# Kernel tuning notes

Measured on AMD Instinct MI355X. Metric: run time of the kernel, lower is better.

## Reference

```python
import jax, jax.numpy as jnp
import numpy as np

B, Q, S, T, H = 8, 64, 64, 64, 768
NH, HD = 12, 64  # head_num, head_dim


def setup_inputs() -> dict:
    key = jax.random.key(0)
    k1, k2, k3, k4, k5, k6, k7 = jax.random.split(key, 7)
    ini_q = jax.random.normal(k1, (B, Q, H), dtype=jnp.float32)
    ini_k = jax.random.normal(k2, (B, S, T, H), dtype=jnp.float32)
    mask = jax.random.randint(k3, (B, S, T), 0, 2).astype(jnp.float32)  # 1 = masked
    # learned params (Linear weights stored as [in, out] for x @ W)
    sc = 1.0 / np.sqrt(H)
    Wq = jax.random.normal(k4, (H, H), dtype=jnp.float32) * sc
    Wkv = jax.random.normal(k5, (H, H), dtype=jnp.float32) * sc
    Wo = jax.random.normal(k6, (H, H), dtype=jnp.float32) * sc
    bo = jax.random.normal(k7, (H,), dtype=jnp.float32) * 0.02
    return {"ini_q": ini_q, "ini_k": ini_k, "mask": mask,
            "Wq": Wq, "Wkv": Wkv, "Wo": Wo, "bo": bo}


def reference(ini_q, ini_k, mask, Wq, Wkv, Wo, bo):
    batch, q_num, _ = ini_q.shape
    _, s_num, t_num, _ = ini_k.shape
    scale = 1.0 / np.sqrt(HD)
    q = (ini_q @ Wq).reshape(batch, q_num, NH, HD)
    kv = (ini_k @ Wkv).reshape(batch, s_num, t_num, NH, HD)  # k == v
    # [b, h, q, s, t]
    scores = jnp.einsum('bqhd,bsthd->bhqst', q, kv) * scale
    scores = scores + mask[:, None, None, :, :] * -10000.0
    alpha = jax.nn.softmax(scores, axis=4)  # dropout is identity in eval
    res = jnp.einsum('bhqst,bsthd->bqshd', alpha, kv).reshape(batch, q_num, s_num, NH * HD)
    return res @ Wo + bo
```

## Files before the change

kernel.cpp:

```cpp
#include <hip/hip_runtime.h>
#include <stdint.h>


typedef __bf16 bf16_t;
typedef __attribute__((ext_vector_type(8))) __bf16 bf16x8;
typedef __attribute__((ext_vector_type(4))) __bf16 bf16x4;
typedef __attribute__((ext_vector_type(4))) float f32x4;

#define HDIM 768

__device__ __forceinline__ void gload16(const bf16_t* g, bf16_t* l) {
  __builtin_amdgcn_global_load_lds(
      (const __attribute__((address_space(1))) void*)g,
      (__attribute__((address_space(3))) void*)l, 16, 0, 0);
}

__global__ __launch_bounds__(256) void splitT3_kernel(
    const float* __restrict__ W0, const float* __restrict__ W1,
    const float* __restrict__ W2,
    bf16_t* __restrict__ h0, bf16_t* __restrict__ l0,
    bf16_t* __restrict__ h1, bf16_t* __restrict__ l1,
    bf16_t* __restrict__ h2, bf16_t* __restrict__ l2) {
  const int kt = blockIdx.x * 64, nt = blockIdx.y * 64, ws = blockIdx.z;
  const float* W = ws == 0 ? W0 : (ws == 1 ? W1 : W2);
  bf16_t* H = ws == 0 ? h0 : (ws == 1 ? h1 : h2);
  bf16_t* L = ws == 0 ? l0 : (ws == 1 ? l1 : l2);
  __shared__ bf16_t Th[64 * 72], Tl[64 * 72];
  const int tid = threadIdx.x;
  const int r0 = tid >> 4, c0 = (tid & 15) * 4;
#pragma unroll
  for (int rg = 0; rg < 4; ++rg) {
    const int r = r0 + rg * 16;
    const float4 v = *(const float4*)&W[(size_t)(kt + r) * HDIM + nt + c0];
    const float vv[4] = {v.x, v.y, v.z, v.w};
#pragma unroll
    for (int e = 0; e < 4; ++e) {
      const bf16_t hb = (bf16_t)vv[e];
      Th[(c0 + e) * 72 + r] = hb;
      Tl[(c0 + e) * 72 + r] = (bf16_t)(vv[e] - (float)hb);
    }
  }
  __syncthreads();
  const int n = tid >> 2, kc = (tid & 3) * 16;
  bf16x8 oh[2], ol[2];
#pragma unroll
  for (int e = 0; e < 16; ++e) {
    oh[e >> 3][e & 7] = Th[n * 72 + kc + e];
    ol[e >> 3][e & 7] = Tl[n * 72 + kc + e];
  }
  const size_t ob = (size_t)(nt + n) * HDIM + kt + kc;
  *(bf16x8*)&H[ob] = oh[0];
  *(bf16x8*)&H[ob + 8] = oh[1];
  *(bf16x8*)&L[ob] = ol[0];
  *(bf16x8*)&L[ob + 8] = ol[1];
}

template <int EPI, bool AF32>
__global__ __launch_bounds__(256) void gemm_kernel(
    const float* __restrict__ Agf,
    const bf16_t* __restrict__ Agh, const bf16_t* __restrict__ Agl,
    const bf16_t* __restrict__ Bgh, const bf16_t* __restrict__ Bgl,
    bf16_t* __restrict__ Ch, bf16_t* __restrict__ Cl,
    bf16_t* __restrict__ CNh, bf16_t* __restrict__ CNl,
    float* __restrict__ Cf, const float* __restrict__ bias) {
  __shared__ bf16_t sAh[128 * 32], sAl[128 * 32];
  __shared__ bf16_t sBh[128 * 32], sBl[128 * 32];
  const int nwg = gridDim.x;
  const int cpx = nwg >> 3;
  const int g = blockIdx.x;
  const int wg = (g & 7) * cpx + (g >> 3);
  const int bn = wg % 6, bm = wg / 6;
  const int tid = threadIdx.x, lane = tid & 63, w = tid >> 6;
  const int wr = (w >> 1) * 64, wc = (w & 1) * 64;
  const int l15 = lane & 15, l4 = lane >> 4;
  f32x4 acc[4][4] = {};

  for (int kt = 0; kt < 24; ++kt) {
    const int k0 = kt * 32;
    __syncthreads();
    if constexpr (AF32) {
#pragma unroll
      for (int j = 0; j < 4; ++j) {
        const int c = tid + j * 256;
        const int row = c >> 3, cg = c & 7;
        const float4 v4 =
            *(const float4*)&Agf[(size_t)(bm * 128 + row) * HDIM + k0 + cg * 4];
        const float vv[4] = {v4.x, v4.y, v4.z, v4.w};
        bf16x4 hv, lv;
#pragma unroll
        for (int e = 0; e < 4; ++e) {
          const bf16_t hb = (bf16_t)vv[e];
          hv[e] = hb;
          lv[e] = (bf16_t)(vv[e] - (float)hb);
        }
        const int off =
            row * 32 + (((cg >> 1) ^ ((row >> 1) & 3)) * 8) + (cg & 1) * 4;
        *(bf16x4*)&sAh[off] = hv;
        *(bf16x4*)&sAl[off] = lv;
      }
    } else {
#pragma unroll
      for (int j = 0; j < 2; ++j) {
        const int c0 = j * 256 + w * 64;
        const int c = c0 + lane;
        const int row = c >> 2, slot = c & 3;
        const size_t ga = (size_t)(bm * 128 + row) * HDIM + k0 +
                          ((slot ^ ((row >> 1) & 3)) * 8);
        gload16(&Agh[ga], &sAh[c0 * 8]);
        gload16(&Agl[ga], &sAl[c0 * 8]);
      }
    }
#pragma unroll
    for (int j = 0; j < 2; ++j) {
      const int c0 = j * 256 + w * 64;
      const int c = c0 + lane;
      const int row = c >> 2, slot = c & 3;
      const size_t gb = (size_t)(bn * 128 + row) * HDIM + k0 +
                        ((slot ^ ((row >> 1) & 3)) * 8);
      gload16(&Bgh[gb], &sBh[c0 * 8]);
      gload16(&Bgl[gb], &sBl[c0 * 8]);
    }
    __syncthreads();
    bf16x8 a_h[4], a_l[4], b_h[4], b_l[4];
#pragma unroll
    for (int m = 0; m < 4; ++m) {
      const int rowa = wr + m * 16 + l15;
      const int ra = rowa * 32 + ((l4 ^ ((rowa >> 1) & 3)) * 8);
      a_h[m] = *(const bf16x8*)&sAh[ra];
      a_l[m] = *(const bf16x8*)&sAl[ra];
      const int rowb = wc + m * 16 + l15;
      const int rb = rowb * 32 + ((l4 ^ ((rowb >> 1) & 3)) * 8);
      b_h[m] = *(const bf16x8*)&sBh[rb];
      b_l[m] = *(const bf16x8*)&sBl[rb];
    }
#pragma unroll
    for (int m = 0; m < 4; ++m)
#pragma unroll
      for (int n = 0; n < 4; ++n) {
        acc[m][n] = __builtin_amdgcn_mfma_f32_16x16x32_bf16(a_h[m], b_h[n], acc[m][n], 0, 0, 0);
        acc[m][n] = __builtin_amdgcn_mfma_f32_16x16x32_bf16(a_h[m], b_l[n], acc[m][n], 0, 0, 0);
        acc[m][n] = __builtin_amdgcn_mfma_f32_16x16x32_bf16(a_l[m], b_h[n], acc[m][n], 0, 0, 0);
      }
  }
#pragma unroll
  for (int m = 0; m < 4; ++m)
#pragma unroll
    for (int n = 0; n < 4; ++n) {
      const int row0 = bm * 128 + wr + m * 16 + l4 * 4;
      const int col = bn * 128 + wc + n * 16 + l15;
      if constexpr (EPI == 1) {
        const float bv = bias[col];
#pragma unroll
        for (int j = 0; j < 4; ++j)
          Cf[(size_t)(row0 + j) * HDIM + col] = acc[m][n][j] + bv;
      } else if constexpr (EPI == 0) {
#pragma unroll
        for (int j = 0; j < 4; ++j) {
          const float v = acc[m][n][j];
          const bf16_t hb = (bf16_t)v;
          Ch[(size_t)(row0 + j) * HDIM + col] = hb;
          Cl[(size_t)(row0 + j) * HDIM + col] = (bf16_t)(v - (float)hb);
        }
      } else {
        const int b = row0 >> 12, s = (row0 >> 6) & 63, t0 = row0 & 63;
        const int hh = col >> 6, d = col & 63;
        const size_t base = ((size_t)((b * 64 + s) * 12 + hh)) * 4096;
#pragma unroll
        for (int j = 0; j < 4; ++j) {
          const float v = acc[m][n][j];
          const bf16_t hb = (bf16_t)v;
          CNh[base + (t0 + j) * 64 + d] = hb;
          CNl[base + (t0 + j) * 64 + d] = (bf16_t)(v - (float)hb);
        }
      }
    }
}

__global__ __launch_bounds__(256, 3) void attn_kernel(
    const bf16_t* __restrict__ qh, const bf16_t* __restrict__ ql,
    const bf16_t* __restrict__ kvNh, const bf16_t* __restrict__ kvNl,
    const float* __restrict__ mask,
    bf16_t* __restrict__ resh, bf16_t* __restrict__ resl) {
  const int sq = blockIdx.x, hh = blockIdx.y, b = blockIdx.z;
  const int s0 = sq * 8;
  const int tid = threadIdx.x, lane = tid & 63, w = tid >> 6;
  const int l15 = lane & 15, l4 = lane >> 4;
  __shared__ bf16_t Kh[64 * 64], Kl[64 * 64];
  __shared__ bf16_t VTh[64 * 72], VTl[64 * 72];
  __shared__ bf16_t Ph[64 * 68], Pl[64 * 68];
  __shared__ float mk[8 * 64];

  {
    const int i2 = tid * 2;
    const float2 mv = *(const float2*)
        &mask[((size_t)(b * 64 + s0 + (i2 >> 6))) * 64 + (i2 & 63)];
    mk[i2] = mv.x * -10000.0f;
    mk[i2 + 1] = mv.y * -10000.0f;
  }

  const size_t qbase = ((size_t)(b * 64 + w * 16 + l15)) * HDIM + hh * 64;
  bf16x8 qf_h[2], qf_l[2];
#pragma unroll
  for (int ks = 0; ks < 2; ++ks) {
    qf_h[ks] = *(const bf16x8*)&qh[qbase + ks * 32 + l4 * 8];
    qf_l[ks] = *(const bf16x8*)&ql[qbase + ks * 32 + l4 * 8];
  }

  const size_t hb0 = ((size_t)((b * 64 + s0) * 12 + hh)) * 4096;
  const size_t SSTR = 12 * 4096;

  bf16x8 nxh[2], nxl[2];
  auto load_next = [&](int sn) {
#pragma unroll
    for (int j = 0; j < 2; ++j) {
      const int c = j * 256 + tid;
      const size_t src = hb0 + (size_t)sn * SSTR + (c >> 3) * 64 + (c & 7) * 8;
      nxh[j] = *(const bf16x8*)&kvNh[src];
      nxl[j] = *(const bf16x8*)&kvNl[src];
    }
  };
  auto write_K = [&]() {
#pragma unroll
    for (int j = 0; j < 2; ++j) {
      const int c = j * 256 + tid;
      const int t = c >> 3, sl = c & 7;
      const int off = t * 64 + ((sl ^ (t & 7)) * 8);
      *(bf16x8*)&Kh[off] = nxh[j];
      *(bf16x8*)&Kl[off] = nxl[j];
    }
  };

  load_next(0);
  write_K();
  __syncthreads();

  const int q = w * 16 + l15;
  for (int si = 0; si < 8; ++si) {
    if (si < 7) load_next(si + 1);

    f32x4 St[4] = {};
#pragma unroll
    for (int ks = 0; ks < 2; ++ks) {
#pragma unroll
      for (int mf = 0; mf < 4; ++mf) {
        const int t = mf * 16 + l15;
        const int off = t * 64 + (((ks * 4 + l4) ^ (t & 7)) * 8);
        const bf16x8 kh8 = *(const bf16x8*)&Kh[off];
        const bf16x8 kl8 = *(const bf16x8*)&Kl[off];
        St[mf] = __builtin_amdgcn_mfma_f32_16x16x32_bf16(kh8, qf_h[ks], St[mf], 0, 0, 0);
        St[mf] = __builtin_amdgcn_mfma_f32_16x16x32_bf16(kh8, qf_l[ks], St[mf], 0, 0, 0);
        St[mf] = __builtin_amdgcn_mfma_f32_16x16x32_bf16(kl8, qf_h[ks], St[mf], 0, 0, 0);
      }
    }

    {
      const int t = lane, sw = t & 7;
#pragma unroll
      for (int ri = 0; ri < 2; ++ri) {
        const int phys = (w * 2 + ri) ^ sw;
        const bf16x8 vh = *(const bf16x8*)&Kh[t * 64 + phys * 8];
        const bf16x8 vl = *(const bf16x8*)&Kl[t * 64 + phys * 8];
        const int d0 = w * 16 + ri * 8;
#pragma unroll
        for (int e = 0; e < 8; ++e) {
          VTh[(d0 + e) * 72 + t] = vh[e];
          VTl[(d0 + e) * 72 + t] = vl[e];
        }
      }
    }

    float p[16];
    float mx = -1e30f;
#pragma unroll
    for (int mf = 0; mf < 4; ++mf)
#pragma unroll
      for (int j = 0; j < 4; ++j) {
        const float v = St[mf][j] * 0.125f + mk[si * 64 + mf * 16 + l4 * 4 + j];
        p[mf * 4 + j] = v;
        mx = fmaxf(mx, v);
      }
    mx = fmaxf(mx, __shfl_xor(mx, 16));
    mx = fmaxf(mx, __shfl_xor(mx, 32));
    float sum = 0.f;
#pragma unroll
    for (int i = 0; i < 16; ++i) {
      const float e = __expf(p[i] - mx);
      p[i] = e;
      sum += e;
    }
    sum += __shfl_xor(sum, 16);
    sum += __shfl_xor(sum, 32);
    const float inv = 1.0f / sum;

#pragma unroll
    for (int mf = 0; mf < 4; ++mf) {
      bf16x4 hv, lv;
#pragma unroll
      for (int j = 0; j < 4; ++j) {
        const float v = p[mf * 4 + j] * inv;
        const bf16_t hb = (bf16_t)v;
        hv[j] = hb;
        lv[j] = (bf16_t)(v - (float)hb);
      }
      *(bf16x4*)&Ph[q * 68 + mf * 16 + l4 * 4] = hv;
      *(bf16x4*)&Pl[q * 68 + mf * 16 + l4 * 4] = lv;
    }
    __syncthreads();

    if (si < 7) write_K();

    f32x4 O[4] = {};
#pragma unroll
    for (int ks = 0; ks < 2; ++ks) {
      const bf16x8 pa = *(const bf16x8*)&Ph[q * 68 + ks * 32 + l4 * 8];
      const bf16x8 pb = *(const bf16x8*)&Pl[q * 68 + ks * 32 + l4 * 8];
#pragma unroll
      for (int nf = 0; nf < 4; ++nf) {
        const int d = nf * 16 + l15;
        const bf16x8 vh = *(const bf16x8*)&VTh[d * 72 + ks * 32 + l4 * 8];
        const bf16x8 vl = *(const bf16x8*)&VTl[d * 72 + ks * 32 + l4 * 8];
        O[nf] = __builtin_amdgcn_mfma_f32_16x16x32_bf16(pa, vh, O[nf], 0, 0, 0);
        O[nf] = __builtin_amdgcn_mfma_f32_16x16x32_bf16(pa, vl, O[nf], 0, 0, 0);
        O[nf] = __builtin_amdgcn_mfma_f32_16x16x32_bf16(pb, vh, O[nf], 0, 0, 0);
      }
    }

#pragma unroll
    for (int nf = 0; nf < 4; ++nf)
#pragma unroll
      for (int j = 0; j < 4; ++j) {
        const int qo = w * 16 + l4 * 4 + j;
        const size_t idx =
            ((size_t)((b * 64 + qo) * 64 + s0 + si)) * HDIM + hh * 64 + nf * 16 + l15;
        const float v = O[nf][j];
        const bf16_t hb = (bf16_t)v;
        resh[idx] = hb;
        resl[idx] = (bf16_t)(v - (float)hb);
      }
    __syncthreads();
  }
}

extern "C" void kernel_launch(void* const* d_in, const int* in_sizes, int n_in,
                              void* d_out, int out_size, void* d_ws, size_t ws_size,
                              hipStream_t stream) {
  const float* ini_q = (const float*)d_in[0];
  const float* ini_k = (const float*)d_in[1];
  const float* mask = (const float*)d_in[2];
  const float* Wq = (const float*)d_in[3];
  const float* Wkv = (const float*)d_in[4];
  const float* Wo = (const float*)d_in[5];
  const float* bo = (const float*)d_in[6];
  float* out = (float*)d_out;

  const size_t SQ = 512ull * HDIM;
  const size_t SK = 32768ull * HDIM;
  const size_t SW = 768ull * HDIM;

  char* p = (char*)d_ws;
  auto carve = [&](size_t bytes) {
    char* r = p;
    p += (bytes + 255) & ~(size_t)255;
    return r;
  };
  bf16_t* wq_h = (bf16_t*)carve(SW * 2);
  bf16_t* wq_l = (bf16_t*)carve(SW * 2);
  bf16_t* wkv_h = (bf16_t*)carve(SW * 2);
  bf16_t* wkv_l = (bf16_t*)carve(SW * 2);
  bf16_t* wo_h = (bf16_t*)carve(SW * 2);
  bf16_t* wo_l = (bf16_t*)carve(SW * 2);
  bf16_t* q_h = (bf16_t*)carve(SQ * 2);
  bf16_t* q_l = (bf16_t*)carve(SQ * 2);
  bf16_t* kvN_h = (bf16_t*)carve(SK * 2);
  bf16_t* kvN_l = (bf16_t*)carve(SK * 2);
  bf16_t* res_h = (bf16_t*)carve(SK * 2);
  bf16_t* res_l = (bf16_t*)carve(SK * 2);
  if ((size_t)(p - (char*)d_ws) > ws_size) return;

  splitT3_kernel<<<dim3(12, 12, 3), 256, 0, stream>>>(
      Wq, Wkv, Wo, wq_h, wq_l, wkv_h, wkv_l, wo_h, wo_l);

  gemm_kernel<0, true><<<dim3(24), 256, 0, stream>>>(
      ini_q, nullptr, nullptr, wq_h, wq_l, q_h, q_l, nullptr, nullptr,
      nullptr, nullptr);
  gemm_kernel<2, true><<<dim3(1536), 256, 0, stream>>>(
      ini_k, nullptr, nullptr, wkv_h, wkv_l, nullptr, nullptr, kvN_h, kvN_l,
      nullptr, nullptr);
  attn_kernel<<<dim3(8, 12, 8), 256, 0, stream>>>(
      q_h, q_l, kvN_h, kvN_l, mask, res_h, res_l);
  gemm_kernel<1, false><<<dim3(1536), 256, 0, stream>>>(
      nullptr, res_h, res_l, wo_h, wo_l, nullptr, nullptr, nullptr, nullptr,
      out, bo);
}
```

Measured before the change: 506.5 us.

## Pre-split fp32 activations to bf16 hi/lo and double-buffer GEMM LDS staging

Adds a standalone split kernel that converts ini_q and ini_k into bf16 hi/lo pairs before the GEMMs, so every GEMM A operand can be loaded straight into LDS with global_load_lds instead of being converted from fp32 inside the k-loop. The GEMM then double-buffers its LDS tiles, issuing the next k-tile's loads before running MFMAs on the current one, with one barrier per iteration. The trade-off is an extra full pass over the large ini_k tensor (read fp32, write two bf16 arrays) and double the GEMM's LDS footprint, which may lower occupancy. The res buffers alias the ik buffers to save workspace; this is safe only because attention runs after the KV GEMM.

```diff
diff --git a/kernel.cpp b/kernel.cpp
--- a/kernel.cpp
+++ b/kernel.cpp
@@ -13,6 +13,23 @@
   __builtin_amdgcn_global_load_lds(
       (const __attribute__((address_space(1))) void*)g,
       (__attribute__((address_space(3))) void*)l, 16, 0, 0);
+}
+
+__global__ __launch_bounds__(256) void split4_kernel(const float* __restrict__ x,
+                                                     bf16_t* __restrict__ h,
+                                                     bf16_t* __restrict__ l) {
+  const int i = blockIdx.x * 256 + threadIdx.x;
+  const float4 v = ((const float4*)x)[i];
+  const float vv[4] = {v.x, v.y, v.z, v.w};
+  bf16x4 hv, lv;
+#pragma unroll
+  for (int e = 0; e < 4; ++e) {
+    const bf16_t hb = (bf16_t)vv[e];
+    hv[e] = hb;
+    lv[e] = (bf16_t)(vv[e] - (float)hb);
+  }
+  ((bf16x4*)h)[i] = hv;
+  ((bf16x4*)l)[i] = lv;
 }
 
 __global__ __launch_bounds__(256) void splitT3_kernel(
@@ -55,16 +72,15 @@
   *(bf16x8*)&L[ob + 8] = ol[1];
 }
 
-template <int EPI, bool AF32>
+template <int EPI>
 __global__ __launch_bounds__(256) void gemm_kernel(
-    const float* __restrict__ Agf,
     const bf16_t* __restrict__ Agh, const bf16_t* __restrict__ Agl,
     const bf16_t* __restrict__ Bgh, const bf16_t* __restrict__ Bgl,
     bf16_t* __restrict__ Ch, bf16_t* __restrict__ Cl,
     bf16_t* __restrict__ CNh, bf16_t* __restrict__ CNl,
     float* __restrict__ Cf, const float* __restrict__ bias) {
-  __shared__ bf16_t sAh[128 * 32], sAl[128 * 32];
-  __shared__ bf16_t sBh[128 * 32], sBl[128 * 32];
+  __shared__ bf16_t sA[2][2][128 * 32];
+  __shared__ bf16_t sB[2][2][128 * 32];
   const int nwg = gridDim.x;
   const int cpx = nwg >> 3;
   const int g = blockIdx.x;
@@ -75,63 +91,40 @@
   const int l15 = lane & 15, l4 = lane >> 4;
   f32x4 acc[4][4] = {};
 
-  for (int kt = 0; kt < 24; ++kt) {
+  auto stage = [&](int buf, int kt) {
     const int k0 = kt * 32;
-    __syncthreads();
-    if constexpr (AF32) {
-#pragma unroll
-      for (int j = 0; j < 4; ++j) {
-        const int c = tid + j * 256;
-        const int row = c >> 3, cg = c & 7;
-        const float4 v4 =
-            *(const float4*)&Agf[(size_t)(bm * 128 + row) * HDIM + k0 + cg * 4];
-        const float vv[4] = {v4.x, v4.y, v4.z, v4.w};
-        bf16x4 hv, lv;
-#pragma unroll
-        for (int e = 0; e < 4; ++e) {
-          const bf16_t hb = (bf16_t)vv[e];
-          hv[e] = hb;
-          lv[e] = (bf16_t)(vv[e] - (float)hb);
-        }
-        const int off =
-            row * 32 + (((cg >> 1) ^ ((row >> 1) & 3)) * 8) + (cg & 1) * 4;
-        *(bf16x4*)&sAh[off] = hv;
-        *(bf16x4*)&sAl[off] = lv;
-      }
-    } else {
-#pragma unroll
-      for (int j = 0; j < 2; ++j) {
-        const int c0 = j * 256 + w * 64;
-        const int c = c0 + lane;
-        const int row = c >> 2, slot = c & 3;
-        const size_t ga = (size_t)(bm * 128 + row) * HDIM + k0 +
-                          ((slot ^ ((row >> 1) & 3)) * 8);
-        gload16(&Agh[ga], &sAh[c0 * 8]);
-        gload16(&Agl[ga], &sAl[c0 * 8]);
-      }
-    }
 #pragma unroll
     for (int j = 0; j < 2; ++j) {
       const int c0 = j * 256 + w * 64;
       const int c = c0 + lane;
       const int row = c >> 2, slot = c & 3;
-      const size_t gb = (size_t)(bn * 128 + row) * HDIM + k0 +
-                        ((slot ^ ((row >> 1) & 3)) * 8);
-      gload16(&Bgh[gb], &sBh[c0 * 8]);
-      gload16(&Bgl[gb], &sBl[c0 * 8]);
-    }
-    __syncthreads();
+      const int soff = ((slot ^ ((row >> 1) & 3)) * 8);
+      const size_t ga = (size_t)(bm * 128 + row) * HDIM + k0 + soff;
+      gload16(&Agh[ga], &sA[buf][0][c0 * 8]);
+      gload16(&Agl[ga], &sA[buf][1][c0 * 8]);
+      const size_t gb = (size_t)(bn * 128 + row) * HDIM + k0 + soff;
+      gload16(&Bgh[gb], &sB[buf][0][c0 * 8]);
+      gload16(&Bgl[gb], &sB[buf][1][c0 * 8]);
+    }
+  };
+
+  stage(0, 0);
+  __syncthreads();
+  int cur = 0;
+
+  for (int kt = 0; kt < 24; ++kt) {
+    if (kt < 23) stage(cur ^ 1, kt + 1);
     bf16x8 a_h[4], a_l[4], b_h[4], b_l[4];
 #pragma unroll
     for (int m = 0; m < 4; ++m) {
       const int rowa = wr + m * 16 + l15;
       const int ra = rowa * 32 + ((l4 ^ ((rowa >> 1) & 3)) * 8);
-      a_h[m] = *(const bf16x8*)&sAh[ra];
-      a_l[m] = *(const bf16x8*)&sAl[ra];
+      a_h[m] = *(const bf16x8*)&sA[cur][0][ra];
+      a_l[m] = *(const bf16x8*)&sA[cur][1][ra];
       const int rowb = wc + m * 16 + l15;
       const int rb = rowb * 32 + ((l4 ^ ((rowb >> 1) & 3)) * 8);
-      b_h[m] = *(const bf16x8*)&sBh[rb];
-      b_l[m] = *(const bf16x8*)&sBl[rb];
+      b_h[m] = *(const bf16x8*)&sB[cur][0][rb];
+      b_l[m] = *(const bf16x8*)&sB[cur][1][rb];
     }
 #pragma unroll
     for (int m = 0; m < 4; ++m)
@@ -141,7 +134,10 @@
         acc[m][n] = __builtin_amdgcn_mfma_f32_16x16x32_bf16(a_h[m], b_l[n], acc[m][n], 0, 0, 0);
         acc[m][n] = __builtin_amdgcn_mfma_f32_16x16x32_bf16(a_l[m], b_h[n], acc[m][n], 0, 0, 0);
       }
-  }
+    __syncthreads();
+    cur ^= 1;
+  }
+
 #pragma unroll
   for (int m = 0; m < 4; ++m)
 #pragma unroll
@@ -363,6 +359,10 @@
     p += (bytes + 255) & ~(size_t)255;
     return r;
   };
+  bf16_t* iq_h = (bf16_t*)carve(SQ * 2);
+  bf16_t* iq_l = (bf16_t*)carve(SQ * 2);
+  bf16_t* ik_h = (bf16_t*)carve(SK * 2);
+  bf16_t* ik_l = (bf16_t*)carve(SK * 2);
   bf16_t* wq_h = (bf16_t*)carve(SW * 2);
   bf16_t* wq_l = (bf16_t*)carve(SW * 2);
   bf16_t* wkv_h = (bf16_t*)carve(SW * 2);
@@ -373,22 +373,21 @@
   bf16_t* q_l = (bf16_t*)carve(SQ * 2);
   bf16_t* kvN_h = (bf16_t*)carve(SK * 2);
   bf16_t* kvN_l = (bf16_t*)carve(SK * 2);
-  bf16_t* res_h = (bf16_t*)carve(SK * 2);
-  bf16_t* res_l = (bf16_t*)carve(SK * 2);
+  bf16_t* res_h = ik_h;
+  bf16_t* res_l = ik_l;
   if ((size_t)(p - (char*)d_ws) > ws_size) return;
 
+  split4_kernel<<<dim3(SQ / 4 / 256), 256, 0, stream>>>(ini_q, iq_h, iq_l);
+  split4_kernel<<<dim3(SK / 4 / 256), 256, 0, stream>>>(ini_k, ik_h, ik_l);
   splitT3_kernel<<<dim3(12, 12, 3), 256, 0, stream>>>(
       Wq, Wkv, Wo, wq_h, wq_l, wkv_h, wkv_l, wo_h, wo_l);
 
-  gemm_kernel<0, true><<<dim3(24), 256, 0, stream>>>(
-      ini_q, nullptr, nullptr, wq_h, wq_l, q_h, q_l, nullptr, nullptr,
-      nullptr, nullptr);
-  gemm_kernel<2, true><<<dim3(1536), 256, 0, stream>>>(
-      ini_k, nullptr, nullptr, wkv_h, wkv_l, nullptr, nullptr, kvN_h, kvN_l,
-      nullptr, nullptr);
+  gemm_kernel<0><<<dim3(24), 256, 0, stream>>>(
+      iq_h, iq_l, wq_h, wq_l, q_h, q_l, nullptr, nullptr, nullptr, nullptr);
+  gemm_kernel<2><<<dim3(1536), 256, 0, stream>>>(
+      ik_h, ik_l, wkv_h, wkv_l, nullptr, nullptr, kvN_h, kvN_l, nullptr, nullptr);
   attn_kernel<<<dim3(8, 12, 8), 256, 0, stream>>>(
       q_h, q_l, kvN_h, kvN_l, mask, res_h, res_l);
-  gemm_kernel<1, false><<<dim3(1536), 256, 0, stream>>>(
-      nullptr, res_h, res_l, wo_h, wo_l, nullptr, nullptr, nullptr, nullptr,
-      out, bo);
-}
+  gemm_kernel<1><<<dim3(1536), 256, 0, stream>>>(
+      res_h, res_l, wo_h, wo_l, nullptr, nullptr, nullptr, nullptr, out, bo);
+}
```

After: 543.8 us. 7.4% more time.
